# Performance work log

Measured on AMD Instinct MI355X. Metric: run time of the kernel, lower is better.

The kernel has to match this reference:

```python
import jax, jax.numpy as jnp
import numpy as np

B, N, M, BUCKETS = 4096, 2048, 2048, 16
T = 100.0  # softmax temperature from module (self.T = 100)


def _make_values(buckets):
    b = buckets // 2
    v = np.zeros((buckets, 1), np.float32)
    for i in range(buckets):
        v[i, 0] = 1.0 / 2.0 ** (b - i) if i < b else -1.0 / 2.0 ** (i - b)
    return jnp.asarray(v)


def setup_inputs() -> dict:
    key = jax.random.key(0)
    ks = jax.random.split(key, 7)
    scale = 1.0 / np.sqrt(M)  # nn.Linear default init range
    return {
        "x": jax.random.normal(ks[0], (B, M), jnp.float32),
        "x_hash": jax.random.normal(ks[1], (B, M), jnp.float32),
        "weight": jax.random.uniform(ks[2], (N, M), jnp.float32, -scale, scale),
        "bias": jax.random.uniform(ks[3], (N,), jnp.float32, -scale, scale),
        "a0": jax.random.normal(ks[4], (BUCKETS, 1), jnp.float32),
        "a1": jax.random.normal(ks[5], (BUCKETS, 1), jnp.float32),
        "a2": jax.random.normal(ks[6], (BUCKETS, 1), jnp.float32),
        "values": _make_values(BUCKETS),
    }


def reference(x, x_hash, weight, bias, a0, a1, a2, values):
    n, m = weight.shape
    fcw = weight.reshape(1, -1)                       # [1, N*M]
    # rank-1 outer products + bias: fx [buckets, N*M]
    fx = a1 @ fcw + a2 @ (fcw * fcw) + a0
    probs = jax.nn.softmax(fx * T, axis=0)            # softmax over buckets
    hash_weight = (probs.T @ values).reshape(n, m)    # [N, M]
    out = x @ weight.T + bias                         # [B, N]
    out_hash = x_hash @ hash_weight.T + bias          # [B, N]
    return out, out_hash
```

## Files before the change

kernel.cpp:

```cpp
#include <hip/hip_runtime.h>
#include <hip/hip_bf16.h>

typedef __attribute__((ext_vector_type(8))) short bf16x8;
typedef __attribute__((ext_vector_type(4))) float f32x4;
typedef __attribute__((ext_vector_type(8))) unsigned short u16x8;
typedef __attribute__((ext_vector_type(4))) unsigned short u16x4;

__device__ __forceinline__ unsigned short f2bf_rtne(float f) {
    unsigned int u = __float_as_uint(f);
    u += 0x7FFFu + ((u >> 16) & 1u);
    return (unsigned short)(u >> 16);
}

__device__ __forceinline__ void gl2lds16(const void* g, void* l) {
    __builtin_amdgcn_global_load_lds((const __attribute__((address_space(1))) void*)g,
                                     (__attribute__((address_space(3))) void*)l, 16, 0, 0);
}

#define NB 16
__global__ void prep_all(const float* __restrict__ x, const float* __restrict__ xh,
                         const float* __restrict__ w,
                         const float* __restrict__ a0, const float* __restrict__ a1,
                         const float* __restrict__ a2, const float* __restrict__ vals,
                         unsigned short* __restrict__ xb, unsigned short* __restrict__ xhb,
                         unsigned short* __restrict__ wbf, unsigned short* __restrict__ hwbf) {
    const int job = blockIdx.y;
    const int stride = gridDim.x * blockDim.x;
    int i = blockIdx.x * blockDim.x + threadIdx.x;
    if (job < 2) {
        const float* in = job ? xh : x;
        unsigned short* out = job ? xhb : xb;
        const int n8 = (4096 * 2048) / 8;
        for (; i < n8; i += stride) {
            const float4* p = (const float4*)in + (size_t)i * 2;
            float4 v0 = p[0];
            float4 v1 = p[1];
            u16x8 r;
            r[0] = f2bf_rtne(v0.x); r[1] = f2bf_rtne(v0.y); r[2] = f2bf_rtne(v0.z); r[3] = f2bf_rtne(v0.w);
            r[4] = f2bf_rtne(v1.x); r[5] = f2bf_rtne(v1.y); r[6] = f2bf_rtne(v1.z); r[7] = f2bf_rtne(v1.w);
            *((u16x8*)out + i) = r;
        }
    } else {
        float A0[NB], A1[NB], A2[NB], V[NB];
#pragma unroll
        for (int b = 0; b < NB; ++b) {
            A0[b] = a0[b] * 100.0f;
            A1[b] = a1[b] * 100.0f;
            A2[b] = a2[b] * 100.0f;
            V[b]  = vals[b];
        }
        const int n4 = (2048 * 2048) / 4;
        for (; i < n4; i += stride) {
            float4 wv = ((const float4*)w)[i];
            float win[4] = {wv.x, wv.y, wv.z, wv.w};
            u16x4 wr, hr;
#pragma unroll
            for (int c = 0; c < 4; ++c) {
                float xx = win[c];
                float x2 = xx * xx;
                float l[NB];
                float mx = -1e30f;
#pragma unroll
                for (int b = 0; b < NB; ++b) {
                    l[b] = fmaf(A1[b], xx, fmaf(A2[b], x2, A0[b]));
                    mx = fmaxf(mx, l[b]);
                }
                float s = 0.0f, acc = 0.0f;
#pragma unroll
                for (int b = 0; b < NB; ++b) {
                    float e = __expf(l[b] - mx);
                    s += e;
                    acc = fmaf(e, V[b], acc);
                }
                wr[c] = f2bf_rtne(xx);
                hr[c] = f2bf_rtne(acc / s);
            }
            *((u16x4*)wbf + i)  = wr;
            *((u16x4*)hwbf + i) = hr;
        }
    }
}

__global__ __launch_bounds__(512, 2) void gemm256(
    const unsigned short* __restrict__ Ax, const unsigned short* __restrict__ Ah,
    const unsigned short* __restrict__ Bw, const unsigned short* __restrict__ Bh,
    const float* __restrict__ bias,
    float* __restrict__ Cx, float* __restrict__ Chh) {
    const int K = 2048, N = 2048;

    __shared__ unsigned short lds[65536];

    const int lin  = blockIdx.x + (blockIdx.y << 4) + (blockIdx.z << 7);
    const int swz  = (lin & 7) * 32 + (lin >> 3);
    const int brow = swz & 15;
    const int bcol = (swz >> 4) & 7;
    const int zz   = swz >> 7;

    const unsigned short* A  = zz ? Ah : Ax;
    const unsigned short* Bm = zz ? Bh : Bw;
    float* C = zz ? Chh : Cx;

    const int tid  = threadIdx.x;
    const int lane = tid & 63;
    const int wid  = tid >> 6;
    const int wr = wid >> 2;
    const int wc = wid & 3;
    const int fr = lane & 15;
    const int fq = lane >> 4;

    const int srow = tid >> 3;
    const int sg8  = ((tid & 7) ^ (srow & 7)) * 8;
    const unsigned short* gA = A  + (size_t)(brow * 256 + srow) * K + sg8;
    const unsigned short* gB = Bm + (size_t)(bcol * 256 + srow) * K + sg8;
    const int wbase = wid * 512;

    const int g0 = (fq ^ (fr & 7)) * 8;
    const int g1 = g0 ^ 32;

#define STAGE_A(buf, h, j) {                                                    \
    const unsigned short* _g = gA + (size_t)((h) * 128) * K + (j) * 64;         \
    gl2lds16(_g,                  lds + (buf) * 16384 + (h) * 8192 + wbase);    \
    gl2lds16(_g + (size_t)64 * K, lds + (buf) * 16384 + (h) * 8192 + 4096 + wbase); }
#define STAGE_B(buf, h, j) {                                                    \
    const unsigned short* _g = gB + (size_t)((h) * 128) * K + (j) * 64;         \
    gl2lds16(_g,                  lds + 32768 + (buf) * 16384 + (h) * 8192 + wbase); \
    gl2lds16(_g + (size_t)64 * K, lds + 32768 + (buf) * 16384 + (h) * 8192 + 4096 + wbase); }

#define LDA(dst, buf, mblk) {                                                   \
    const unsigned short* _p = lds + (buf) * 16384 + (wr * 128 + (mblk) * 16 + fr) * 64; \
    dst[0] = *(const bf16x8*)(_p + g0);                                         \
    dst[1] = *(const bf16x8*)(_p + g1); }
#define LDB(dst, buf, nblk) {                                                   \
    const unsigned short* _p = lds + 32768 + (buf) * 16384 + (wc * 64 + (nblk) * 16 + fr) * 64; \
    dst[0] = *(const bf16x8*)(_p + g0);                                         \
    dst[1] = *(const bf16x8*)(_p + g1); }

#define MM(mi, n, kk, AF) acc[mi][n] = __builtin_amdgcn_mfma_f32_16x16x32_bf16(AF[kk], bfr[n][kk], acc[mi][n], 0, 0, 0)

#define PHASE(q, buf, STG, GATE) {                                              \
    if ((q) == 0) {                                                             \
        LDB(bfr[0], buf, 0); LDB(bfr[1], buf, 1);                               \
        LDB(bfr[2], buf, 2); LDB(bfr[3], buf, 3);                               \
    }                                                                           \
    LDA(af0, buf, 2 * (q)); LDA(af1, buf, 2 * (q) + 1);                         \
    STG;                                                                        \
    if ((q) == 0) asm volatile("s_waitcnt lgkmcnt(8)" ::: "memory");            \
    __builtin_amdgcn_s_barrier();                                               \
    asm volatile("s_waitcnt lgkmcnt(0)" ::: "memory");                          \
    __builtin_amdgcn_s_setprio(1);                                              \
    MM(2*(q),0,0,af0); MM(2*(q)+1,0,0,af1); MM(2*(q),1,0,af0); MM(2*(q)+1,1,0,af1); \
    MM(2*(q),2,0,af0); MM(2*(q)+1,2,0,af1); MM(2*(q),3,0,af0); MM(2*(q)+1,3,0,af1); \
    MM(2*(q),0,1,af0); MM(2*(q)+1,0,1,af1); MM(2*(q),1,1,af0); MM(2*(q)+1,1,1,af1); \
    MM(2*(q),2,1,af0); MM(2*(q)+1,2,1,af1); MM(2*(q),3,1,af0); MM(2*(q)+1,3,1,af1); \
    __builtin_amdgcn_s_setprio(0);                                              \
    GATE;                                                                       \
    __builtin_amdgcn_s_barrier(); }

    STAGE_A(0, 0, 0); STAGE_A(0, 1, 0);
    STAGE_B(0, 0, 0); STAGE_B(0, 1, 0);
    STAGE_B(1, 0, 1); STAGE_B(1, 1, 1);
    asm volatile("s_waitcnt vmcnt(4)" ::: "memory");
    __builtin_amdgcn_s_barrier();

    f32x4 acc[8][4] = {};
    bf16x8 bfr[4][2], af0[2], af1[2];

#pragma unroll 1
    for (int t = 0; t < 15; ++t) {
        const int j1 = 2 * t + 1, j2 = 2 * t + 2, j3 = 2 * t + 3;
        PHASE(0, 0, STAGE_A(1, 0, j1), );
        PHASE(1, 0, STAGE_A(1, 1, j1), );
        PHASE(2, 0, STAGE_B(0, 0, j2), );
        PHASE(3, 0, STAGE_B(0, 1, j2), asm volatile("s_waitcnt vmcnt(4)" ::: "memory"));
        PHASE(0, 1, STAGE_A(0, 0, j2), );
        PHASE(1, 1, STAGE_A(0, 1, j2), );
        PHASE(2, 1, STAGE_B(1, 0, j3), );
        PHASE(3, 1, STAGE_B(1, 1, j3), asm volatile("s_waitcnt vmcnt(4)" ::: "memory"));
    }
    PHASE(0, 0, STAGE_A(1, 0, 31), );
    PHASE(1, 0, STAGE_A(1, 1, 31), );
    PHASE(2, 0, , );
    PHASE(3, 0, , asm volatile("s_waitcnt vmcnt(0)" ::: "memory"));
    PHASE(0, 1, , );
    PHASE(1, 1, , );
    PHASE(2, 1, , );
    PHASE(3, 1, , );

#pragma unroll
    for (int n = 0; n < 4; ++n) {
        const int col = bcol * 256 + wc * 64 + n * 16 + fr;
        const float bv = bias[col];
#pragma unroll
        for (int m = 0; m < 8; ++m) {
            const int row0 = brow * 256 + wr * 128 + m * 16 + fq * 4;
#pragma unroll
            for (int r = 0; r < 4; ++r)
                C[(size_t)(row0 + r) * N + col] = acc[m][n][r] + bv;
        }
    }
#undef STAGE_A
#undef STAGE_B
#undef LDA
#undef LDB
#undef MM
#undef PHASE
}

extern "C" void kernel_launch(void* const* d_in, const int* in_sizes, int n_in,
                              void* d_out, int out_size, void* d_ws, size_t ws_size,
                              hipStream_t stream) {
    const float* x    = (const float*)d_in[0];
    const float* xh   = (const float*)d_in[1];
    const float* w    = (const float*)d_in[2];
    const float* bias = (const float*)d_in[3];
    const float* a0   = (const float*)d_in[4];
    const float* a1   = (const float*)d_in[5];
    const float* a2   = (const float*)d_in[6];
    const float* vals = (const float*)d_in[7];

    float* out  = (float*)d_out;
    float* outh = out + (size_t)4096 * 2048;

    char* ws = (char*)d_ws;
    unsigned short* xb  = (unsigned short*)(ws);
    unsigned short* xhb = (unsigned short*)(ws + (size_t)16 * 1024 * 1024);
    unsigned short* wb  = (unsigned short*)(ws + (size_t)32 * 1024 * 1024);
    unsigned short* hwb = (unsigned short*)(ws + (size_t)40 * 1024 * 1024);

    prep_all<<<dim3(1024, 3), 256, 0, stream>>>(x, xh, w, a0, a1, a2, vals, xb, xhb, wb, hwb);

    dim3 grid(4096 / 256, 2048 / 256, 2);
    gemm256<<<grid, 512, 0, stream>>>(xb, xhb, wb, hwb, bias, out, outh);
}
```

Before: 103.3 us.

## Fuse fp32-to-bf16 activation conversion into GEMM A-tile loading

Drops the separate prep pass that converted x and x_hash to bf16 and instead loads fp32 A tiles into registers inside the GEMM, converting and writing them to swizzled LDS. This avoids writing and re-reading the bf16 activation copies and one launch's worth of work. In exchange, A now moves through registers instead of direct global-to-LDS loads, reads twice the bytes per element, repeats the conversion in every column block, and raises register pressure with a reshuffled wait/barrier schedule.

After: 113.2 us. 1.1x slower.

```diff
diff --git a/kernel.cpp b/kernel.cpp
--- a/kernel.cpp
+++ b/kernel.cpp
@@ -18,71 +18,52 @@
 }
 
 #define NB 16
-__global__ void prep_all(const float* __restrict__ x, const float* __restrict__ xh,
-                         const float* __restrict__ w,
-                         const float* __restrict__ a0, const float* __restrict__ a1,
-                         const float* __restrict__ a2, const float* __restrict__ vals,
-                         unsigned short* __restrict__ xb, unsigned short* __restrict__ xhb,
-                         unsigned short* __restrict__ wbf, unsigned short* __restrict__ hwbf) {
-    const int job = blockIdx.y;
+__global__ void hash_prep(const float* __restrict__ w,
+                          const float* __restrict__ a0, const float* __restrict__ a1,
+                          const float* __restrict__ a2, const float* __restrict__ vals,
+                          unsigned short* __restrict__ wbf, unsigned short* __restrict__ hwbf) {
+    float A0[NB], A1[NB], A2[NB], V[NB];
+#pragma unroll
+    for (int b = 0; b < NB; ++b) {
+        A0[b] = a0[b] * 100.0f;
+        A1[b] = a1[b] * 100.0f;
+        A2[b] = a2[b] * 100.0f;
+        V[b]  = vals[b];
+    }
+    const int n4 = (2048 * 2048) / 4;
     const int stride = gridDim.x * blockDim.x;
-    int i = blockIdx.x * blockDim.x + threadIdx.x;
-    if (job < 2) {
-        const float* in = job ? xh : x;
-        unsigned short* out = job ? xhb : xb;
-        const int n8 = (4096 * 2048) / 8;
-        for (; i < n8; i += stride) {
-            const float4* p = (const float4*)in + (size_t)i * 2;
-            float4 v0 = p[0];
-            float4 v1 = p[1];
-            u16x8 r;
-            r[0] = f2bf_rtne(v0.x); r[1] = f2bf_rtne(v0.y); r[2] = f2bf_rtne(v0.z); r[3] = f2bf_rtne(v0.w);
-            r[4] = f2bf_rtne(v1.x); r[5] = f2bf_rtne(v1.y); r[6] = f2bf_rtne(v1.z); r[7] = f2bf_rtne(v1.w);
-            *((u16x8*)out + i) = r;
+    for (int i = blockIdx.x * blockDim.x + threadIdx.x; i < n4; i += stride) {
+        float4 wv = ((const float4*)w)[i];
+        float win[4] = {wv.x, wv.y, wv.z, wv.w};
+        u16x4 wr, hr;
+#pragma unroll
+        for (int c = 0; c < 4; ++c) {
+            float xx = win[c];
+            float x2 = xx * xx;
+            float l[NB];
+            float mx = -1e30f;
+#pragma unroll
+            for (int b = 0; b < NB; ++b) {
+                l[b] = fmaf(A1[b], xx, fmaf(A2[b], x2, A0[b]));
+                mx = fmaxf(mx, l[b]);
+            }
+            float s = 0.0f, acc = 0.0f;
+#pragma unroll
+            for (int b = 0; b < NB; ++b) {
+                float e = __expf(l[b] - mx);
+                s += e;
+                acc = fmaf(e, V[b], acc);
+            }
+            wr[c] = f2bf_rtne(xx);
+            hr[c] = f2bf_rtne(acc / s);
         }
-    } else {
-        float A0[NB], A1[NB], A2[NB], V[NB];
-#pragma unroll
-        for (int b = 0; b < NB; ++b) {
-            A0[b] = a0[b] * 100.0f;
-            A1[b] = a1[b] * 100.0f;
-            A2[b] = a2[b] * 100.0f;
-            V[b]  = vals[b];
-        }
-        const int n4 = (2048 * 2048) / 4;
-        for (; i < n4; i += stride) {
-            float4 wv = ((const float4*)w)[i];
-            float win[4] = {wv.x, wv.y, wv.z, wv.w};
-            u16x4 wr, hr;
-#pragma unroll
-            for (int c = 0; c < 4; ++c) {
-                float xx = win[c];
-                float x2 = xx * xx;
-                float l[NB];
-                float mx = -1e30f;
-#pragma unroll
-                for (int b = 0; b < NB; ++b) {
-                    l[b] = fmaf(A1[b], xx, fmaf(A2[b], x2, A0[b]));
-                    mx = fmaxf(mx, l[b]);
-                }
-                float s = 0.0f, acc = 0.0f;
-#pragma unroll
-                for (int b = 0; b < NB; ++b) {
-                    float e = __expf(l[b] - mx);
-                    s += e;
-                    acc = fmaf(e, V[b], acc);
-                }
-                wr[c] = f2bf_rtne(xx);
-                hr[c] = f2bf_rtne(acc / s);
-            }
-            *((u16x4*)wbf + i)  = wr;
-            *((u16x4*)hwbf + i) = hr;
-        }
+        *((u16x4*)wbf + i)  = wr;
+        *((u16x4*)hwbf + i) = hr;
     }
 }
 
 __global__ __launch_bounds__(512, 2) void gemm256(
-    const unsigned short* __restrict__ Ax, const unsigned short* __restrict__ Ah,
+    const float* __restrict__ Axf, const float* __restrict__ Ahf,
     const unsigned short* __restrict__ Bw, const unsigned short* __restrict__ Bh,
     const float* __restrict__ bias,
     float* __restrict__ Cx, float* __restrict__ Chh) {
@@ -96,7 +77,7 @@
     const int bcol = (swz >> 4) & 7;
     const int zz   = swz >> 7;
 
-    const unsigned short* A  = zz ? Ah : Ax;
+    const float* Af = zz ? Ahf : Axf;
     const unsigned short* Bm = zz ? Bh : Bw;
     float* C = zz ? Chh : Cx;
 
@@ -109,18 +90,37 @@
     const int fq = lane >> 4;
 
     const int srow = tid >> 3;
-    const int sg8  = ((tid & 7) ^ (srow & 7)) * 8;
-    const unsigned short* gA = A  + (size_t)(brow * 256 + srow) * K + sg8;
+    const float* gAf = Af + (size_t)(brow * 256 + srow) * K + (tid & 7) * 8;
+    const int aswz = ((tid & 7) ^ (srow & 7)) * 8;
+
+    const int sg8 = ((tid & 7) ^ (srow & 7)) * 8;
     const unsigned short* gB = Bm + (size_t)(bcol * 256 + srow) * K + sg8;
     const int wbase = wid * 512;
 
     const int g0 = (fq ^ (fr & 7)) * 8;
     const int g1 = g0 ^ 32;
 
-#define STAGE_A(buf, h, j) {                                                    \
-    const unsigned short* _g = gA + (size_t)((h) * 128) * K + (j) * 64;         \
-    gl2lds16(_g,                  lds + (buf) * 16384 + (h) * 8192 + wbase);    \
-    gl2lds16(_g + (size_t)64 * K, lds + (buf) * 16384 + (h) * 8192 + 4096 + wbase); }
+#define LOAD_A(R, h, j) {                                                       \
+    const float* _p = gAf + (size_t)(h) * 128 * K + (j) * 64;                   \
+    R[0] = *(const float4*)(_p);                                                \
+    R[1] = *(const float4*)(_p + 4);                                            \
+    R[2] = *(const float4*)(_p + (size_t)64 * K);                               \
+    R[3] = *(const float4*)(_p + (size_t)64 * K + 4); }
+
+#define WRITE_A(R, buf, h) {                                                    \
+    unsigned short* _d = lds + (buf) * 16384 + (h) * 8192 + srow * 64 + aswz;   \
+    u16x8 _v0, _v1;                                                             \
+    _v0[0] = f2bf_rtne(R[0].x); _v0[1] = f2bf_rtne(R[0].y);                     \
+    _v0[2] = f2bf_rtne(R[0].z); _v0[3] = f2bf_rtne(R[0].w);                     \
+    _v0[4] = f2bf_rtne(R[1].x); _v0[5] = f2bf_rtne(R[1].y);                     \
+    _v0[6] = f2bf_rtne(R[1].z); _v0[7] = f2bf_rtne(R[1].w);                     \
+    _v1[0] = f2bf_rtne(R[2].x); _v1[1] = f2bf_rtne(R[2].y);                     \
+    _v1[2] = f2bf_rtne(R[2].z); _v1[3] = f2bf_rtne(R[2].w);                     \
+    _v1[4] = f2bf_rtne(R[3].x); _v1[5] = f2bf_rtne(R[3].y);                     \
+    _v1[6] = f2bf_rtne(R[3].z); _v1[7] = f2bf_rtne(R[3].w);                     \
+    *(u16x8*)_d = _v0;                                                          \
+    *(u16x8*)(_d + 4096) = _v1; }
+
 #define STAGE_B(buf, h, j) {                                                    \
     const unsigned short* _g = gB + (size_t)((h) * 128) * K + (j) * 64;         \
     gl2lds16(_g,                  lds + 32768 + (buf) * 16384 + (h) * 8192 + wbase); \
@@ -144,7 +144,6 @@
     }                                                                           \
     LDA(af0, buf, 2 * (q)); LDA(af1, buf, 2 * (q) + 1);                         \
     STG;                                                                        \
-    if ((q) == 0) asm volatile("s_waitcnt lgkmcnt(8)" ::: "memory");            \
     __builtin_amdgcn_s_barrier();                                               \
     asm volatile("s_waitcnt lgkmcnt(0)" ::: "memory");                          \
     __builtin_amdgcn_s_setprio(1);                                              \
@@ -156,10 +155,17 @@
     GATE;                                                                       \
     __builtin_amdgcn_s_barrier(); }
 
-    STAGE_A(0, 0, 0); STAGE_A(0, 1, 0);
+    float4 aP[4], aQ[4];
+
+    LOAD_A(aP, 0, 0);
+    LOAD_A(aQ, 1, 0);
     STAGE_B(0, 0, 0); STAGE_B(0, 1, 0);
     STAGE_B(1, 0, 1); STAGE_B(1, 1, 1);
-    asm volatile("s_waitcnt vmcnt(4)" ::: "memory");
+    WRITE_A(aP, 0, 0);
+    WRITE_A(aQ, 0, 1);
+    LOAD_A(aP, 0, 1);
+    asm volatile("s_waitcnt vmcnt(8)" ::: "memory");
+    asm volatile("s_waitcnt lgkmcnt(0)" ::: "memory");
     __builtin_amdgcn_s_barrier();
 
     f32x4 acc[8][4] = {};
@@ -168,17 +174,17 @@
 #pragma unroll 1
     for (int t = 0; t < 15; ++t) {
         const int j1 = 2 * t + 1, j2 = 2 * t + 2, j3 = 2 * t + 3;
-        PHASE(0, 0, STAGE_A(1, 0, j1), );
-        PHASE(1, 0, STAGE_A(1, 1, j1), );
-        PHASE(2, 0, STAGE_B(0, 0, j2), );
-        PHASE(3, 0, STAGE_B(0, 1, j2), asm volatile("s_waitcnt vmcnt(4)" ::: "memory"));
-        PHASE(0, 1, STAGE_A(0, 0, j2), );
-        PHASE(1, 1, STAGE_A(0, 1, j2), );
-        PHASE(2, 1, STAGE_B(1, 0, j3), );
-        PHASE(3, 1, STAGE_B(1, 1, j3), asm volatile("s_waitcnt vmcnt(4)" ::: "memory"));
-    }
-    PHASE(0, 0, STAGE_A(1, 0, 31), );
-    PHASE(1, 0, STAGE_A(1, 1, 31), );
+        PHASE(0, 0, { WRITE_A(aP, 1, 0); LOAD_A(aQ, 1, j1); }, );
+        PHASE(1, 0, { WRITE_A(aQ, 1, 1); }, );
+        PHASE(2, 0, { STAGE_B(0, 0, j2); }, );
+        PHASE(3, 0, { LOAD_A(aP, 0, j2); STAGE_B(0, 1, j2); }, );
+        PHASE(0, 1, { WRITE_A(aP, 0, 0); LOAD_A(aQ, 1, j2); }, );
+        PHASE(1, 1, { WRITE_A(aQ, 0, 1); }, );
+        PHASE(2, 1, { STAGE_B(1, 0, j3); }, );
+        PHASE(3, 1, { LOAD_A(aP, 0, j3); STAGE_B(1, 1, j3); }, );
+    }
+    PHASE(0, 0, { WRITE_A(aP, 1, 0); LOAD_A(aQ, 1, 31); }, );
+    PHASE(1, 0, { WRITE_A(aQ, 1, 1); }, );
     PHASE(2, 0, , );
     PHASE(3, 0, , asm volatile("s_waitcnt vmcnt(0)" ::: "memory"));
     PHASE(0, 1, , );
@@ -198,7 +204,8 @@
                 C[(size_t)(row0 + r) * N + col] = acc[m][n][r] + bv;
         }
     }
-#undef STAGE_A
+#undef LOAD_A
+#undef WRITE_A
 #undef STAGE_B
 #undef LDA
 #undef LDB
@@ -222,13 +229,11 @@
     float* outh = out + (size_t)4096 * 2048;
 
     char* ws = (char*)d_ws;
-    unsigned short* xb  = (unsigned short*)(ws);
-    unsigned short* xhb = (unsigned short*)(ws + (size_t)16 * 1024 * 1024);
-    unsigned short* wb  = (unsigned short*)(ws + (size_t)32 * 1024 * 1024);
-    unsigned short* hwb = (unsigned short*)(ws + (size_t)40 * 1024 * 1024);
-
-    prep_all<<<dim3(1024, 3), 256, 0, stream>>>(x, xh, w, a0, a1, a2, vals, xb, xhb, wb, hwb);
+    unsigned short* wb  = (unsigned short*)(ws);
+    unsigned short* hwb = (unsigned short*)(ws + (size_t)8 * 1024 * 1024);
+
+    hash_prep<<<1024, 256, 0, stream>>>(w, a0, a1, a2, vals, wb, hwb);
 
     dim3 grid(4096 / 256, 2048 / 256, 2);
-    gemm256<<<grid, 512, 0, stream>>>(xb, xhb, wb, hwb, bias, out, outh);
-}
+    gemm256<<<grid, 512, 0, stream>>>(x, xh, wb, hwb, bias, out, outh);
+}
```
